# Performance work log

Hardware: AMD Instinct MI355X
Metric: run time of the kernel (lower is better)

## Reference

```python
import jax, jax.numpy as jnp
import numpy as np

N, M, D = 32768, 8192, 64

def setup_inputs() -> dict:
    key = jax.random.key(0)
    k1, k2, k3 = jax.random.split(key, 3)
    inputx = jax.random.normal(k1, (N, D), dtype=jnp.float32)
    y = jax.random.normal(k2, (M, D), dtype=jnp.float32)
    # psi is initialized to zeros in the module, but use random values so the
    # dual-variable subtraction actually affects the argmin/min.
    psi = jax.random.normal(k3, (M,), dtype=jnp.float32)
    return {"inputx": inputx, "y": y, "psi": psi}

def reference(inputx, y, psi):
    # cxy[i,j] = ||x_i||^2 + ||y_j||^2 - 2 <x_i, y_j>   (squared euclidean cost)
    x2 = jnp.sum(inputx * inputx, axis=1, keepdims=True)          # [N,1]
    y2 = jnp.sum(y * y, axis=1)[None, :]                          # [1,M]
    cxy = x2 + y2 - 2.0 * jnp.matmul(inputx, y.T)                 # [N,M]
    # semi-dual: mean_i min_j (c(x_i,y_j) - psi_j) + mean_j psi_j
    loss = jnp.mean(jnp.min(cxy - psi[None, :], axis=1)) + jnp.mean(psi)
    return loss
```

## Files before the change

### kernel.cpp

```cpp
#include <hip/hip_runtime.h>

#define N_ROWS 32768
#define M_COLS 8192
#define D_DIM  64
#define JC     8
#define PBLOCK 256
#define BLOCK  256
#define RBLOCK 128
#define GROUPS 2
#define ROWS_PER_BLOCK 256
#define CHUNK  (M_COLS / JC)
#define TJ     128
#define NTILE  (CHUNK / TJ)

typedef _Float16 v8h  __attribute__((ext_vector_type(8)));
typedef _Float16 v4h  __attribute__((ext_vector_type(4)));
typedef float    v4f  __attribute__((ext_vector_type(4)));
typedef float    v16f __attribute__((ext_vector_type(16)));

__global__ __launch_bounds__(PBLOCK) void prep_kernel(
    const float* __restrict__ y, const float* __restrict__ psi,
    const float* __restrict__ x, _Float16* __restrict__ yh,
    float* __restrict__ th, _Float16* __restrict__ xh,
    float* __restrict__ x2, float* __restrict__ out) {
    const int tid = threadIdx.x;
    const int bid = blockIdx.x;
    const int n = tid & 15;
    if (bid < M_COLS / 16) {
        if (bid == 0 && tid == 0) out[0] = 0.f;
        const int j = bid * 16 + (tid >> 4);
        const float4 v = *(const float4*)(y + (size_t)j * D_DIM + n * 4);
        float s = v.x * v.x + v.y * v.y + v.z * v.z + v.w * v.w;
        v4h hv = { (_Float16)v.x, (_Float16)v.y, (_Float16)v.z, (_Float16)v.w };
        *(v4h*)(yh + (size_t)j * D_DIM + n * 4) = hv;
#pragma unroll
        for (int m = 1; m < 16; m <<= 1) s += __shfl_xor(s, m, 64);
        if (n == 0) th[j] = 0.5f * (psi[j] - s);
    } else {
        const int i = (bid - M_COLS / 16) * 16 + (tid >> 4);
        const float4 v = *(const float4*)(x + (size_t)i * D_DIM + n * 4);
        float s = v.x * v.x + v.y * v.y + v.z * v.z + v.w * v.w;
        v4h hv = { (_Float16)v.x, (_Float16)v.y, (_Float16)v.z, (_Float16)v.w };
        *(v4h*)(xh + (size_t)i * D_DIM + n * 4) = hv;
#pragma unroll
        for (int m = 1; m < 16; m <<= 1) s += __shfl_xor(s, m, 64);
        if (n == 0) x2[i] = s;
    }
}

__global__ __launch_bounds__(BLOCK, 2) void partial_min_kernel(
    const _Float16* __restrict__ xh, const _Float16* __restrict__ yh,
    const float* __restrict__ th, float* __restrict__ part) {
    __shared__ __align__(16) _Float16 sY[2][TJ * D_DIM];
    __shared__ __align__(16) float    sTh[2][TJ];

    const int tid  = threadIdx.x;
    const int lane = tid & 63, wave = tid >> 6;
    const int hi = lane >> 5, r32 = lane & 31;
    const int jc    = blockIdx.y;
    const int jbase = jc * CHUNK;
    const int i_wave = blockIdx.x * ROWS_PER_BLOCK + wave * (GROUPS * 32);

    auto stage = [&](int t, int b) {
#pragma unroll
        for (int k = 0; k < 4; ++k) {
            const int sIdx = (k * 4 + wave) * 64 + lane;
            const int row  = sIdx >> 3;
            const int c    = (sIdx & 7) ^ (row & 7);
            const _Float16* g = yh + (size_t)(jbase + t * TJ + row) * D_DIM + c * 8;
            __builtin_amdgcn_global_load_lds(
                (const __attribute__((address_space(1))) void*)g,
                (__attribute__((address_space(3))) void*)(&sY[b][(size_t)(k * 4 + wave) * 512]),
                16, 0, 0);
        }
        if (wave == 0 && lane < 32) {
            const float* gt_ = th + (size_t)(jbase + t * TJ) + lane * 4;
            __builtin_amdgcn_global_load_lds(
                (const __attribute__((address_space(1))) void*)gt_,
                (__attribute__((address_space(3))) void*)(&sTh[b][0]),
                16, 0, 0);
        }
    };

    stage(0, 0);

    v8h a[GROUPS][4];
#pragma unroll
    for (int g = 0; g < GROUPS; ++g) {
        const _Float16* px = xh + (size_t)(i_wave + g * 32 + r32) * D_DIM + hi * 8;
#pragma unroll
        for (int ks = 0; ks < 4; ++ks) a[g][ks] = *(const v8h*)(px + ks * 16);
    }

    v16f vmax[GROUPS];
#pragma unroll
    for (int g = 0; g < GROUPS; ++g)
#pragma unroll
        for (int e = 0; e < 16; ++e) vmax[g][e] = -INFINITY;

    const int boff0 = r32 * 128 + (((0 * 2 + hi) ^ (r32 & 7)) * 16);
    const int boff1 = r32 * 128 + (((1 * 2 + hi) ^ (r32 & 7)) * 16);
    const int boff2 = r32 * 128 + (((2 * 2 + hi) ^ (r32 & 7)) * 16);
    const int boff3 = r32 * 128 + (((3 * 2 + hi) ^ (r32 & 7)) * 16);

    __syncthreads();

    for (int t = 0; t < NTILE; ++t) {
        const int cur = t & 1;
        if (t + 1 < NTILE) stage(t + 1, cur ^ 1);

        const char*  buf  = (const char*)&sY[cur][0];
        const float* tbuf = &sTh[cur][0];
#pragma unroll
        for (int jb = 0; jb < TJ / 32; ++jb) {
            const v8h b0 = *(const v8h*)(buf + jb * 4096 + boff0);
            const v8h b1 = *(const v8h*)(buf + jb * 4096 + boff1);
            const v8h b2 = *(const v8h*)(buf + jb * 4096 + boff2);
            const v8h b3 = *(const v8h*)(buf + jb * 4096 + boff3);
            const float tl = tbuf[jb * 32 + r32];
            v16f cin;
#pragma unroll
            for (int e = 0; e < 16; ++e) cin[e] = tl;
            __builtin_amdgcn_s_setprio(1);
#pragma unroll
            for (int g = 0; g < GROUPS; ++g) {
                v16f acc = __builtin_amdgcn_mfma_f32_32x32x16_f16(a[g][0], b0, cin, 0, 0, 0);
                acc = __builtin_amdgcn_mfma_f32_32x32x16_f16(a[g][1], b1, acc, 0, 0, 0);
                acc = __builtin_amdgcn_mfma_f32_32x32x16_f16(a[g][2], b2, acc, 0, 0, 0);
                acc = __builtin_amdgcn_mfma_f32_32x32x16_f16(a[g][3], b3, acc, 0, 0, 0);
#pragma unroll
                for (int e = 0; e < 16; ++e)
                    vmax[g][e] = fmaxf(vmax[g][e], acc[e]);
            }
            __builtin_amdgcn_s_setprio(0);
        }
        __syncthreads();
    }

#pragma unroll
    for (int g = 0; g < GROUPS; ++g) {
#pragma unroll
        for (int e = 0; e < 16; ++e) {
            float v = vmax[g][e];
#pragma unroll
            for (int m = 1; m < 32; m <<= 1)
                v = fmaxf(v, __shfl_xor(v, m, 64));
            vmax[g][e] = v;
        }
        float v = vmax[g][0];
#pragma unroll
        for (int e = 1; e < 16; ++e) v = (r32 == e) ? vmax[g][e] : v;
        if (r32 < 16)
            part[(size_t)jc * N_ROWS + i_wave + g * 32
                 + (r32 & 3) + 8 * (r32 >> 2) + 4 * hi] = -2.f * v;
    }
}

__global__ __launch_bounds__(RBLOCK) void reduce_kernel(
    const float* __restrict__ part, const float* __restrict__ x2,
    const float* __restrict__ psi, float* __restrict__ out) {
    const int tid = threadIdx.x;
    const int gt  = blockIdx.x * RBLOCK + tid;
    float m = part[gt];
#pragma unroll
    for (int c = 1; c < JC; ++c)
        m = fminf(m, part[(size_t)c * N_ROWS + gt]);
    float s = (m + x2[gt]) * (1.f / (float)N_ROWS);
    if (gt < M_COLS) s += psi[gt] * (1.f / (float)M_COLS);
    for (int off = 32; off > 0; off >>= 1) s += __shfl_down(s, off, 64);
    __shared__ float tmp[2];
    if ((tid & 63) == 0) tmp[tid >> 6] = s;
    __syncthreads();
    if (tid == 0) atomicAdd(out, tmp[0] + tmp[1]);
}

extern "C" void kernel_launch(void* const* d_in, const int* in_sizes, int n_in,
                              void* d_out, int out_size, void* d_ws, size_t ws_size,
                              hipStream_t stream) {
    const float* x   = (const float*)d_in[0];
    const float* y   = (const float*)d_in[1];
    const float* psi = (const float*)d_in[2];
    float* out = (float*)d_out;

    float* part = (float*)d_ws;
    float* th   = part + (size_t)JC * N_ROWS;
    float* x2   = th + (size_t)M_COLS;
    _Float16* yh = (_Float16*)(x2 + (size_t)N_ROWS);
    _Float16* xh = yh + (size_t)M_COLS * D_DIM;

    prep_kernel<<<(M_COLS + N_ROWS) / 16, PBLOCK, 0, stream>>>(y, psi, x, yh, th, xh, x2, out);
    partial_min_kernel<<<dim3(N_ROWS / ROWS_PER_BLOCK, JC), BLOCK, 0, stream>>>(xh, yh, th, part);
    reduce_kernel<<<N_ROWS / RBLOCK, RBLOCK, 0, stream>>>(part, x2, psi, out);
}
```

Before: 105.1 us.

## Triple-buffer Y tiles with vmcnt waits and a stronger LDS swizzle

Moves from double to triple buffering of the Y/threshold tiles in LDS, prefetching two tiles ahead and replacing the per-tile __syncthreads with a manual s_waitcnt vmcnt plus barrier at the top of each tile, so global-to-LDS loads overlap more with MFMA work. Extends the XOR swizzle with extra row bits to reduce LDS bank conflicts on the B-operand reads. Every wave now issues the threshold load, and the tile loop is fully unrolled. The added buffer raises LDS use, which may limit occupancy, and the hand-counted vmcnt(5) is fragile: it assumes a fixed number of outstanding loads per wave.

```diff
diff --git a/kernel.cpp b/kernel.cpp
--- a/kernel.cpp
+++ b/kernel.cpp
@@ -12,6 +12,7 @@
 #define CHUNK  (M_COLS / JC)
 #define TJ     128
 #define NTILE  (CHUNK / TJ)
+#define NBUF   3
 
 typedef _Float16 v8h  __attribute__((ext_vector_type(8)));
 typedef _Float16 v4h  __attribute__((ext_vector_type(4)));
@@ -51,8 +52,8 @@
 __global__ __launch_bounds__(BLOCK, 2) void partial_min_kernel(
     const _Float16* __restrict__ xh, const _Float16* __restrict__ yh,
     const float* __restrict__ th, float* __restrict__ part) {
-    __shared__ __align__(16) _Float16 sY[2][TJ * D_DIM];
-    __shared__ __align__(16) float    sTh[2][TJ];
+    __shared__ __align__(16) _Float16 sY[NBUF][TJ * D_DIM];
+    __shared__ __align__(16) float    sTh[NBUF][TJ];
 
     const int tid  = threadIdx.x;
     const int lane = tid & 63, wave = tid >> 6;
@@ -66,14 +67,14 @@
         for (int k = 0; k < 4; ++k) {
             const int sIdx = (k * 4 + wave) * 64 + lane;
             const int row  = sIdx >> 3;
-            const int c    = (sIdx & 7) ^ (row & 7);
+            const int c    = (sIdx & 7) ^ (row & 7) ^ ((((row >> 3) & 3)) << 1);
             const _Float16* g = yh + (size_t)(jbase + t * TJ + row) * D_DIM + c * 8;
             __builtin_amdgcn_global_load_lds(
                 (const __attribute__((address_space(1))) void*)g,
                 (__attribute__((address_space(3))) void*)(&sY[b][(size_t)(k * 4 + wave) * 512]),
                 16, 0, 0);
         }
-        if (wave == 0 && lane < 32) {
+        if (lane < 32) {
             const float* gt_ = th + (size_t)(jbase + t * TJ) + lane * 4;
             __builtin_amdgcn_global_load_lds(
                 (const __attribute__((address_space(1))) void*)gt_,
@@ -92,25 +93,31 @@
         for (int ks = 0; ks < 4; ++ks) a[g][ks] = *(const v8h*)(px + ks * 16);
     }
 
+    stage(1, 1);
+
     v16f vmax[GROUPS];
 #pragma unroll
     for (int g = 0; g < GROUPS; ++g)
 #pragma unroll
         for (int e = 0; e < 16; ++e) vmax[g][e] = -INFINITY;
 
-    const int boff0 = r32 * 128 + (((0 * 2 + hi) ^ (r32 & 7)) * 16);
-    const int boff1 = r32 * 128 + (((1 * 2 + hi) ^ (r32 & 7)) * 16);
-    const int boff2 = r32 * 128 + (((2 * 2 + hi) ^ (r32 & 7)) * 16);
-    const int boff3 = r32 * 128 + (((3 * 2 + hi) ^ (r32 & 7)) * 16);
-
-    __syncthreads();
-
+    const int sw = (r32 & 7) ^ (((r32 >> 3) & 3) << 1);
+    const int boff0 = r32 * 128 + (((0 * 2 + hi) ^ sw) * 16);
+    const int boff1 = r32 * 128 + (((1 * 2 + hi) ^ sw) * 16);
+    const int boff2 = r32 * 128 + (((2 * 2 + hi) ^ sw) * 16);
+    const int boff3 = r32 * 128 + (((3 * 2 + hi) ^ sw) * 16);
+
+#pragma unroll
     for (int t = 0; t < NTILE; ++t) {
-        const int cur = t & 1;
-        if (t + 1 < NTILE) stage(t + 1, cur ^ 1);
-
-        const char*  buf  = (const char*)&sY[cur][0];
-        const float* tbuf = &sTh[cur][0];
+        if (t < NTILE - 1) asm volatile("s_waitcnt vmcnt(5)" ::: "memory");
+        else               asm volatile("s_waitcnt vmcnt(0)" ::: "memory");
+        __builtin_amdgcn_s_barrier();
+        asm volatile("" ::: "memory");
+
+        if (t + 2 < NTILE) stage(t + 2, (t + 2) % NBUF);
+
+        const char*  buf  = (const char*)&sY[t % NBUF][0];
+        const float* tbuf = &sTh[t % NBUF][0];
 #pragma unroll
         for (int jb = 0; jb < TJ / 32; ++jb) {
             const v8h b0 = *(const v8h*)(buf + jb * 4096 + boff0);
@@ -134,7 +141,6 @@
             }
             __builtin_amdgcn_s_setprio(0);
         }
-        __syncthreads();
     }
 
 #pragma unroll
```

After: 317.4 us. 3.02x slower.

## Load Y tiles directly from global memory instead of staging through LDS

Applied to the files above, without the earlier changes.

Removes the double-buffered LDS staging of Y and theta, along with its barriers, so each wave reads its B fragments and theta values straight from global memory (L1/L2) in a loop unrolled by two. The goal is to drop the per-tile synchronization and LDS traffic. In exchange, the B reads become per-lane 16-byte global loads that are less coalesced, and waves in a block redundantly fetch the same Y data. Latency is now hidden only by the unroll and by occupancy.

```diff
diff --git a/kernel.cpp b/kernel.cpp
--- a/kernel.cpp
+++ b/kernel.cpp
@@ -10,12 +10,9 @@
 #define GROUPS 2
 #define ROWS_PER_BLOCK 256
 #define CHUNK  (M_COLS / JC)
-#define TJ     128
-#define NTILE  (CHUNK / TJ)
 
 typedef _Float16 v8h  __attribute__((ext_vector_type(8)));
 typedef _Float16 v4h  __attribute__((ext_vector_type(4)));
-typedef float    v4f  __attribute__((ext_vector_type(4)));
 typedef float    v16f __attribute__((ext_vector_type(16)));
 
 __global__ __launch_bounds__(PBLOCK) void prep_kernel(
@@ -51,38 +48,12 @@
 __global__ __launch_bounds__(BLOCK, 2) void partial_min_kernel(
     const _Float16* __restrict__ xh, const _Float16* __restrict__ yh,
     const float* __restrict__ th, float* __restrict__ part) {
-    __shared__ __align__(16) _Float16 sY[2][TJ * D_DIM];
-    __shared__ __align__(16) float    sTh[2][TJ];
-
     const int tid  = threadIdx.x;
     const int lane = tid & 63, wave = tid >> 6;
     const int hi = lane >> 5, r32 = lane & 31;
     const int jc    = blockIdx.y;
     const int jbase = jc * CHUNK;
     const int i_wave = blockIdx.x * ROWS_PER_BLOCK + wave * (GROUPS * 32);
-
-    auto stage = [&](int t, int b) {
-#pragma unroll
-        for (int k = 0; k < 4; ++k) {
-            const int sIdx = (k * 4 + wave) * 64 + lane;
-            const int row  = sIdx >> 3;
-            const int c    = (sIdx & 7) ^ (row & 7);
-            const _Float16* g = yh + (size_t)(jbase + t * TJ + row) * D_DIM + c * 8;
-            __builtin_amdgcn_global_load_lds(
-                (const __attribute__((address_space(1))) void*)g,
-                (__attribute__((address_space(3))) void*)(&sY[b][(size_t)(k * 4 + wave) * 512]),
-                16, 0, 0);
-        }
-        if (wave == 0 && lane < 32) {
-            const float* gt_ = th + (size_t)(jbase + t * TJ) + lane * 4;
-            __builtin_amdgcn_global_load_lds(
-                (const __attribute__((address_space(1))) void*)gt_,
-                (__attribute__((address_space(3))) void*)(&sTh[b][0]),
-                16, 0, 0);
-        }
-    };
-
-    stage(0, 0);
 
     v8h a[GROUPS][4];
 #pragma unroll
@@ -98,43 +69,32 @@
 #pragma unroll
         for (int e = 0; e < 16; ++e) vmax[g][e] = -INFINITY;
 
-    const int boff0 = r32 * 128 + (((0 * 2 + hi) ^ (r32 & 7)) * 16);
-    const int boff1 = r32 * 128 + (((1 * 2 + hi) ^ (r32 & 7)) * 16);
-    const int boff2 = r32 * 128 + (((2 * 2 + hi) ^ (r32 & 7)) * 16);
-    const int boff3 = r32 * 128 + (((3 * 2 + hi) ^ (r32 & 7)) * 16);
+    const _Float16* yb = yh + (size_t)(jbase + r32) * D_DIM + hi * 8;
+    const float*    tb = th + jbase + r32;
 
-    __syncthreads();
-
-    for (int t = 0; t < NTILE; ++t) {
-        const int cur = t & 1;
-        if (t + 1 < NTILE) stage(t + 1, cur ^ 1);
-
-        const char*  buf  = (const char*)&sY[cur][0];
-        const float* tbuf = &sTh[cur][0];
+#pragma unroll 2
+    for (int jj = 0; jj < CHUNK / 32; ++jj) {
+        const _Float16* yr = yb + (size_t)jj * 32 * D_DIM;
+        const v8h b0 = *(const v8h*)(yr);
+        const v8h b1 = *(const v8h*)(yr + 16);
+        const v8h b2 = *(const v8h*)(yr + 32);
+        const v8h b3 = *(const v8h*)(yr + 48);
+        const float tl = tb[jj * 32];
+        v16f cin;
 #pragma unroll
-        for (int jb = 0; jb < TJ / 32; ++jb) {
-            const v8h b0 = *(const v8h*)(buf + jb * 4096 + boff0);
-            const v8h b1 = *(const v8h*)(buf + jb * 4096 + boff1);
-            const v8h b2 = *(const v8h*)(buf + jb * 4096 + boff2);
-            const v8h b3 = *(const v8h*)(buf + jb * 4096 + boff3);
-            const float tl = tbuf[jb * 32 + r32];
-            v16f cin;
+        for (int e = 0; e < 16; ++e) cin[e] = tl;
+        __builtin_amdgcn_s_setprio(1);
 #pragma unroll
-            for (int e = 0; e < 16; ++e) cin[e] = tl;
-            __builtin_amdgcn_s_setprio(1);
+        for (int g = 0; g < GROUPS; ++g) {
+            v16f acc = __builtin_amdgcn_mfma_f32_32x32x16_f16(a[g][0], b0, cin, 0, 0, 0);
+            acc = __builtin_amdgcn_mfma_f32_32x32x16_f16(a[g][1], b1, acc, 0, 0, 0);
+            acc = __builtin_amdgcn_mfma_f32_32x32x16_f16(a[g][2], b2, acc, 0, 0, 0);
+            acc = __builtin_amdgcn_mfma_f32_32x32x16_f16(a[g][3], b3, acc, 0, 0, 0);
 #pragma unroll
-            for (int g = 0; g < GROUPS; ++g) {
-                v16f acc = __builtin_amdgcn_mfma_f32_32x32x16_f16(a[g][0], b0, cin, 0, 0, 0);
-                acc = __builtin_amdgcn_mfma_f32_32x32x16_f16(a[g][1], b1, acc, 0, 0, 0);
-                acc = __builtin_amdgcn_mfma_f32_32x32x16_f16(a[g][2], b2, acc, 0, 0, 0);
-                acc = __builtin_amdgcn_mfma_f32_32x32x16_f16(a[g][3], b3, acc, 0, 0, 0);
-#pragma unroll
-                for (int e = 0; e < 16; ++e)
-                    vmax[g][e] = fmaxf(vmax[g][e], acc[e]);
-            }
-            __builtin_amdgcn_s_setprio(0);
+            for (int e = 0; e < 16; ++e)
+                vmax[g][e] = fmaxf(vmax[g][e], acc[e]);
         }
-        __syncthreads();
+        __builtin_amdgcn_s_setprio(0);
     }
 
 #pragma unroll
```

After: 135.3 us. +28.7%, slower.
